# Optimization experiments

Measured on AMD Instinct MI355X. Metric: run time of the kernel, lower is better.

The kernel has to match this reference:

```python
import jax, jax.numpy as jnp
import numpy as np

B, S, EMBED_DIM, FFN_DIM, N_QUBITS = 8, 4096, 768, 3072, 8

# Quantum math: each qubit starts in |0>, gets RX(x_i) then RY(theta_i), then <Z_i>.
# Since all gates are single-qubit, qubits are independent; a short derivation gives
#   <Z_i> = cos(x_i) * cos(theta_i)
# (RX(phi)|0> = (cos(phi/2), -i sin(phi/2)); apply RY(theta); |a|^2-|b|^2 = cos(theta)cos(phi)).

def setup_inputs() -> dict:
    key = jax.random.key(0)
    k1, k2, k3, k4 = jax.random.split(key, 4)
    x = jax.random.normal(k1, (B, S, EMBED_DIM), dtype=jnp.float32)
    theta = jax.random.normal(k2, (N_QUBITS,), dtype=jnp.float32)  # trainable RY angles
    W1 = jax.random.normal(k3, (FFN_DIM, N_QUBITS), dtype=jnp.float32) / np.sqrt(N_QUBITS)
    W2 = jax.random.normal(k4, (EMBED_DIM, FFN_DIM), dtype=jnp.float32) / np.sqrt(FFN_DIM)
    return {"x": x, "theta": theta, "W1": W1, "W2": W2}


def reference(x, theta, W1, W2):
    # RX-encode first N_QUBITS features of each token, RY params, PauliZ expectation.
    # Closed form of the product-state circuit: z[b,s,q] = cos(x[b,s,q]) * cos(theta[q])
    z = jnp.cos(x[..., :N_QUBITS]) * jnp.cos(theta)            # [B, S, Q]
    # dropout is identity in eval mode
    h = jax.nn.relu(jnp.einsum("bsq,fq->bsf", z, W1))          # [B, S, F]
    out = jnp.einsum("bsf,ef->bse", h, W2)                     # [B, S, E]
    return out
```

## Files before the change

kernel.cpp:

```cpp
#include <hip/hip_runtime.h>
#include <hip/hip_bf16.h>
#include <math.h>

#define T_TOK   32768
#define EDIM    768
#define FDIM    3072
#define NQ      8

#define NET     24
#define NKF     192
#define NFT     96
#define NTT     1024

#define NMB     128
#define NPAN    6

#define W2P_BYTES (NKF * NET * 64 * 8 * 2)
#define W1P_BYTES (NFT * 64 * 8 * 2)
#define ZP_BYTES  (NTT * 64 * 8 * 2)
#define W1P_OFFU  (W2P_BYTES / 2)
#define ZP_OFFU   ((W2P_BYTES + W1P_BYTES) / 2)
#define WS_NEED   ((size_t)(W2P_BYTES + W1P_BYTES + ZP_BYTES))

typedef float f32x16 __attribute__((ext_vector_type(16)));
typedef float f32x4  __attribute__((ext_vector_type(4)));
typedef short bf16x8 __attribute__((ext_vector_type(8)));

union FragU { uint4 u; bf16x8 v; };

static __device__ __forceinline__ unsigned pack2(float lo, float hi) {
    unsigned r;
    asm("v_cvt_pk_bf16_f32 %0, %1, %2" : "=v"(r) : "v"(lo), "v"(hi));
    return r;
}

static __device__ __forceinline__ unsigned short f2bf(float f) {
    unsigned int u = __float_as_uint(f);
    unsigned int r = (u + 0x7FFFu + ((u >> 16) & 1u)) >> 16;
    return (unsigned short)r;
}

__global__ __launch_bounds__(256) void ffq_pack(
    const float* __restrict__ x, const float* __restrict__ theta,
    const float* __restrict__ W1, const float* __restrict__ W2,
    unsigned short* __restrict__ ws)
{
    const int bid = blockIdx.x;
    unsigned short* W2P = ws;
    unsigned short* W1P = ws + W1P_OFFU;
    unsigned short* ZP  = ws + ZP_OFFU;

    if (bid < 1152) {
        const int t = bid * 256 + threadIdx.x;
        const int lane = t & 63, fe = t >> 6;
        const int kf = fe / NET, et = fe - kf * NET;
        const int g = lane >> 5, c = lane & 31;
        const int e  = et * 32 + c;
        const int f0 = kf * 16 + g * 4;
        const float4 a = *(const float4*)(W2 + (size_t)e * FDIM + f0);
        const float4 b = *(const float4*)(W2 + (size_t)e * FDIM + f0 + 8);
        FragU u;
        u.u.x = pack2(a.x, a.y); u.u.y = pack2(a.z, a.w);
        u.u.z = pack2(b.x, b.y); u.u.w = pack2(b.z, b.w);
        *(uint4*)(W2P + (((size_t)et * NKF + kf) * 64 + lane) * 8) = u.u;
    } else if (bid < 1176) {
        const int t = (bid - 1152) * 256 + threadIdx.x;
        const int lane = t & 63, ft = t >> 6;
        const int g = lane >> 5, c = lane & 31;
        FragU u; u.u = (uint4){0, 0, 0, 0};
        if (g == 0) {
            const float4 a = *(const float4*)(W1 + (size_t)(ft * 32 + c) * NQ);
            const float4 b = *(const float4*)(W1 + (size_t)(ft * 32 + c) * NQ + 4);
            u.u.x = pack2(a.x, a.y); u.u.y = pack2(a.z, a.w);
            u.u.z = pack2(b.x, b.y); u.u.w = pack2(b.z, b.w);
        }
        *(uint4*)(W1P + (size_t)t * 8) = u.u;
    } else {
        const int t = (bid - 1176) * 256 + threadIdx.x;
        const int lane = t & 63, tt = t >> 6;
        const int g = lane >> 5, c = lane & 31;
        FragU u; u.u = (uint4){0, 0, 0, 0};
        if (g == 0) {
            const int token = tt * 32 + c;
            const float4 a = *(const float4*)(x + (size_t)token * EDIM);
            const float4 b = *(const float4*)(x + (size_t)token * EDIM + 4);
            const float z0 = __cosf(a.x) * __cosf(theta[0]);
            const float z1 = __cosf(a.y) * __cosf(theta[1]);
            const float z2 = __cosf(a.z) * __cosf(theta[2]);
            const float z3 = __cosf(a.w) * __cosf(theta[3]);
            const float z4 = __cosf(b.x) * __cosf(theta[4]);
            const float z5 = __cosf(b.y) * __cosf(theta[5]);
            const float z6 = __cosf(b.z) * __cosf(theta[6]);
            const float z7 = __cosf(b.w) * __cosf(theta[7]);
            u.u.x = pack2(z0, z1); u.u.y = pack2(z2, z3);
            u.u.z = pack2(z4, z5); u.u.w = pack2(z6, z7);
        }
        *(uint4*)(ZP + (size_t)t * 8) = u.u;
    }
}

#define SGB(mask, n) __builtin_amdgcn_sched_group_barrier((mask), (n), 0)

__global__ __launch_bounds__(256, 2) void ffq_main(
    const unsigned short* __restrict__ ws, float* __restrict__ out)
{
    const unsigned short* W1Pp = ws + W1P_OFFU;
    const unsigned short* ZP   = ws + ZP_OFFU;

    const int tid  = threadIdx.x;
    const int wave = tid >> 6;
    const int lane = tid & 63;
    const int g    = lane >> 5;
    const int c    = lane & 31;

    const int sw    = (blockIdx.x & 7) * 96 + (blockIdx.x >> 3);
    const int panel = sw / NMB;
    const int mblk  = sw % NMB;

    const int tt0 = mblk * 8 + wave * 2;
    const int et0 = panel * 4;
    const size_t lo8 = (size_t)lane * 8;

    const bf16x8 zb0 = *(const bf16x8*)(ZP + (size_t)tt0 * 512 + lo8);
    const bf16x8 zb1 = *(const bf16x8*)(ZP + (size_t)(tt0 + 1) * 512 + lo8);

    const unsigned lane16 = (unsigned)lane * 16u;
    const unsigned vo0 = (unsigned)((et0 + 0) * NKF) * 1024u + lane16;
    const unsigned vo1 = (unsigned)((et0 + 1) * NKF) * 1024u + lane16;
    const unsigned vo2 = (unsigned)((et0 + 2) * NKF) * 1024u + lane16;
    const unsigned vo3 = (unsigned)((et0 + 3) * NKF) * 1024u + lane16;
    const char* Wb = (const char*)ws;

    const f32x16 Zc = (f32x16)(0.f);
    f32x16 A00 = Zc, A01 = Zc, A02 = Zc, A03 = Zc;
    f32x16 A10 = Zc, A11 = Zc, A12 = Zc, A13 = Zc;
    f32x16 d0, d1;
    bf16x8 a0l, a0h, a1l, a1h;
    bf16x8 Bl0, Bl1, Bl2, Bl3, Bh0, Bh1, Bh2, Bh3;
    bf16x8 wa;

#define MFMA32(A, B, C) __builtin_amdgcn_mfma_f32_32x32x16_bf16((A), (B), (C), 0, 0, 0)

#define MKAF(d, o) ({                                                    \
        FragU u_;                                                        \
        u_.u.x = pack2(fmaxf((d)[(o)+0], 0.f), fmaxf((d)[(o)+1], 0.f));  \
        u_.u.y = pack2(fmaxf((d)[(o)+2], 0.f), fmaxf((d)[(o)+3], 0.f));  \
        u_.u.z = pack2(fmaxf((d)[(o)+4], 0.f), fmaxf((d)[(o)+5], 0.f));  \
        u_.u.w = pack2(fmaxf((d)[(o)+6], 0.f), fmaxf((d)[(o)+7], 0.f));  \
        u_.v; })

    Bl0 = *(const bf16x8*)(Wb + vo0);        Bh0 = *(const bf16x8*)(Wb + vo0 + 1024);
    Bl1 = *(const bf16x8*)(Wb + vo1);        Bh1 = *(const bf16x8*)(Wb + vo1 + 1024);
    Bl2 = *(const bf16x8*)(Wb + vo2);        Bh2 = *(const bf16x8*)(Wb + vo2 + 1024);
    Bl3 = *(const bf16x8*)(Wb + vo3);        Bh3 = *(const bf16x8*)(Wb + vo3 + 1024);
    wa  = *(const bf16x8*)(W1Pp + lo8);
    d0 = MFMA32(wa, zb0, Zc);
    d1 = MFMA32(wa, zb1, Zc);
    wa  = *(const bf16x8*)(W1Pp + 512 + lo8);
    a0l = MKAF(d0, 0); a0h = MKAF(d0, 8);
    a1l = MKAF(d1, 0); a1h = MKAF(d1, 8);

    #pragma unroll 1
    for (int n = 0; n < NFT; ++n) {
        d0 = MFMA32(wa, zb0, Zc);
        d1 = MFMA32(wa, zb1, Zc);
        wa = *(const bf16x8*)(W1Pp + (size_t)(n + 2) * 512 + lo8);

        A00 = MFMA32(a0l, Bl0, A00); A01 = MFMA32(a0l, Bl1, A01);
        A02 = MFMA32(a0l, Bl2, A02); A03 = MFMA32(a0l, Bl3, A03);
        A10 = MFMA32(a1l, Bl0, A10); A11 = MFMA32(a1l, Bl1, A11);
        A12 = MFMA32(a1l, Bl2, A12); A13 = MFMA32(a1l, Bl3, A13);
        Bl0 = *(const bf16x8*)(Wb + vo0 + 2048);
        Bl1 = *(const bf16x8*)(Wb + vo1 + 2048);
        Bl2 = *(const bf16x8*)(Wb + vo2 + 2048);
        Bl3 = *(const bf16x8*)(Wb + vo3 + 2048);
        a0l = MKAF(d0, 0);
        a1l = MKAF(d1, 0);
        SGB(0x8, 2); SGB(0x20, 1);
        SGB(0x8, 2); SGB(0x20, 1); SGB(0x2, 6);
        SGB(0x8, 2); SGB(0x20, 1); SGB(0x2, 6);
        SGB(0x8, 2); SGB(0x20, 1); SGB(0x2, 6);
        SGB(0x8, 2); SGB(0x20, 1); SGB(0x2, 6);

        A00 = MFMA32(a0h, Bh0, A00); A01 = MFMA32(a0h, Bh1, A01);
        A02 = MFMA32(a0h, Bh2, A02); A03 = MFMA32(a0h, Bh3, A03);
        A10 = MFMA32(a1h, Bh0, A10); A11 = MFMA32(a1h, Bh1, A11);
        A12 = MFMA32(a1h, Bh2, A12); A13 = MFMA32(a1h, Bh3, A13);
        Bh0 = *(const bf16x8*)(Wb + vo0 + 3072);
        Bh1 = *(const bf16x8*)(Wb + vo1 + 3072);
        Bh2 = *(const bf16x8*)(Wb + vo2 + 3072);
        Bh3 = *(const bf16x8*)(Wb + vo3 + 3072);
        a0h = MKAF(d0, 8);
        a1h = MKAF(d1, 8);
        SGB(0x8, 2); SGB(0x20, 1); SGB(0x2, 6);
        SGB(0x8, 2); SGB(0x20, 1); SGB(0x2, 6);
        SGB(0x8, 2); SGB(0x20, 1); SGB(0x2, 6);
        SGB(0x8, 2); SGB(0x20, 1); SGB(0x2, 6);

        Wb += 2048;
    }

#define STORE_ACC(ACC, T, E) do {                                              \
        const size_t rb = (size_t)((tt0 + (T)) * 32 + 4 * g) * EDIM            \
                          + (size_t)(et0 + (E)) * 32 + c;                      \
        _Pragma("unroll")                                                      \
        for (int r = 0; r < 16; ++r)                                           \
            out[rb + (size_t)((r & 3) + 8 * (r >> 2)) * EDIM] = ACC[r];        \
    } while (0)

    STORE_ACC(A00, 0, 0); STORE_ACC(A01, 0, 1); STORE_ACC(A02, 0, 2); STORE_ACC(A03, 0, 3);
    STORE_ACC(A10, 1, 0); STORE_ACC(A11, 1, 1); STORE_ACC(A12, 1, 2); STORE_ACC(A13, 1, 3);

#undef MFMA32
#undef MKAF
#undef STORE_ACC
}

#define BM      128
#define NPANEL  6
#define NMBLK   256
#define BK      64
#define NKSTEP  (FDIM / BK)
#define HA_ST   72
#define BT_ST   72

__global__ __launch_bounds__(256) void ffq_fused(
    const float* __restrict__ x, const float* __restrict__ theta,
    const float* __restrict__ W1, const float* __restrict__ W2,
    float* __restrict__ out)
{
    __shared__ __align__(16) unsigned short hA[BM * HA_ST];
    __shared__ __align__(16) unsigned short Bt[BM * BT_ST];

    const int tid  = threadIdx.x;
    const int wave = tid >> 6;
    const int lane = tid & 63;
    const int l15  = lane & 15;
    const int lhi  = lane >> 4;
    const int wm   = wave >> 1;
    const int wn   = wave & 1;

    const int panel = blockIdx.x / NMBLK;
    const int mblk  = blockIdx.x % NMBLK;
    const int t0 = mblk * BM;
    const int n0 = panel * BM;

    bf16x8 zf[2];
    #pragma unroll
    for (int s = 0; s < 2; ++s) {
        bf16x8 z = {0, 0, 0, 0, 0, 0, 0, 0};
        if (lhi == 0) {
            const int tok = t0 + (wave * 2 + s) * 16 + l15;
            const float4* xp = (const float4*)(x + (size_t)tok * EDIM);
            const float4 x0 = xp[0];
            const float4 x1 = xp[1];
            z[0] = (short)f2bf(cosf(x0.x) * cosf(theta[0]));
            z[1] = (short)f2bf(cosf(x0.y) * cosf(theta[1]));
            z[2] = (short)f2bf(cosf(x0.z) * cosf(theta[2]));
            z[3] = (short)f2bf(cosf(x0.w) * cosf(theta[3]));
            z[4] = (short)f2bf(cosf(x1.x) * cosf(theta[4]));
            z[5] = (short)f2bf(cosf(x1.y) * cosf(theta[5]));
            z[6] = (short)f2bf(cosf(x1.z) * cosf(theta[6]));
            z[7] = (short)f2bf(cosf(x1.w) * cosf(theta[7]));
        }
        zf[s] = z;
    }

    f32x4 acc[4][4];
    #pragma unroll
    for (int mi = 0; mi < 4; ++mi)
        #pragma unroll
        for (int ni = 0; ni < 4; ++ni)
            acc[mi][ni] = (f32x4){0.f, 0.f, 0.f, 0.f};

    for (int ks = 0; ks < NKSTEP; ++ks) {
        const int k0 = ks * BK;
        __syncthreads();
        {
            const int e    = tid >> 1;
            const int half = (tid & 1) * 32;
            const float* src = W2 + (size_t)(n0 + e) * FDIM + k0 + half;
            unsigned short* dst = &Bt[e * BT_ST + half];
            #pragma unroll
            for (int i = 0; i < 4; ++i) {
                const float4 a = ((const float4*)src)[2 * i];
                const float4 b = ((const float4*)src)[2 * i + 1];
                bf16x8 v;
                v[0] = (short)f2bf(a.x); v[1] = (short)f2bf(a.y);
                v[2] = (short)f2bf(a.z); v[3] = (short)f2bf(a.w);
                v[4] = (short)f2bf(b.x); v[5] = (short)f2bf(b.y);
                v[6] = (short)f2bf(b.z); v[7] = (short)f2bf(b.w);
                *(bf16x8*)(dst + i * 8) = v;
            }
        }
        #pragma unroll
        for (int ns = 0; ns < 4; ++ns) {
            bf16x8 wf = {0, 0, 0, 0, 0, 0, 0, 0};
            if (lhi == 0) {
                const float* wp = W1 + (size_t)(k0 + ns * 16 + l15) * NQ;
                const float4 a = ((const float4*)wp)[0];
                const float4 b = ((const float4*)wp)[1];
                wf[0] = (short)f2bf(a.x); wf[1] = (short)f2bf(a.y);
                wf[2] = (short)f2bf(a.z); wf[3] = (short)f2bf(a.w);
                wf[4] = (short)f2bf(b.x); wf[5] = (short)f2bf(b.y);
                wf[6] = (short)f2bf(b.z); wf[7] = (short)f2bf(b.w);
            }
            #pragma unroll
            for (int s = 0; s < 2; ++s) {
                f32x4 hd = __builtin_amdgcn_mfma_f32_16x16x32_bf16(
                    zf[s], wf, (f32x4){0.f, 0.f, 0.f, 0.f}, 0, 0, 0);
                const int row = (wave * 2 + s) * 16 + lhi * 4;
                const int col = ns * 16 + l15;
                #pragma unroll
                for (int j = 0; j < 4; ++j) {
                    const float v = hd[j] > 0.f ? hd[j] : 0.f;
                    hA[(row + j) * HA_ST + col] = f2bf(v);
                }
            }
        }
        __syncthreads();
        #pragma unroll
        for (int ksub = 0; ksub < 2; ++ksub) {
            bf16x8 af[4], bg[4];
            #pragma unroll
            for (int mi = 0; mi < 4; ++mi) {
                const int row = wm * 64 + mi * 16 + l15;
                af[mi] = *(const bf16x8*)&hA[row * HA_ST + ksub * 32 + lhi * 8];
            }
            #pragma unroll
            for (int ni = 0; ni < 4; ++ni) {
                const int e = wn * 64 + ni * 16 + l15;
                bg[ni] = *(const bf16x8*)&Bt[e * BT_ST + ksub * 32 + lhi * 8];
            }
            #pragma unroll
            for (int mi = 0; mi < 4; ++mi)
                #pragma unroll
                for (int ni = 0; ni < 4; ++ni)
                    acc[mi][ni] = __builtin_amdgcn_mfma_f32_16x16x32_bf16(
                        af[mi], bg[ni], acc[mi][ni], 0, 0, 0);
        }
    }

    #pragma unroll
    for (int mi = 0; mi < 4; ++mi) {
        const int rbase = t0 + wm * 64 + mi * 16 + lhi * 4;
        #pragma unroll
        for (int ni = 0; ni < 4; ++ni) {
            const int cc = n0 + wn * 64 + ni * 16 + l15;
            #pragma unroll
            for (int j = 0; j < 4; ++j)
                out[(size_t)(rbase + j) * EDIM + cc] = acc[mi][ni][j];
        }
    }
}

extern "C" void kernel_launch(void* const* d_in, const int* in_sizes, int n_in,
                              void* d_out, int out_size, void* d_ws, size_t ws_size,
                              hipStream_t stream) {
    const float* x     = (const float*)d_in[0];
    const float* theta = (const float*)d_in[1];
    const float* W1    = (const float*)d_in[2];
    const float* W2    = (const float*)d_in[3];
    float* out = (float*)d_out;

    if (ws_size >= WS_NEED) {
        ffq_pack<<<dim3(1432), dim3(256), 0, stream>>>(x, theta, W1, W2,
                                                       (unsigned short*)d_ws);
        ffq_main<<<dim3(NPAN * NMB), dim3(256), 0, stream>>>(
            (const unsigned short*)d_ws, out);
    } else {
        ffq_fused<<<dim3(NPANEL * NMBLK), dim3(256), 0, stream>>>(x, theta, W1, W2, out);
    }
}
```

Measured before the change: 157.0 us.

## Stage W2 and W1 tiles through double-buffered LDS via global_load_lds

Replaces the per-wave direct global loads of W2 B-fragments and W1 fragments with a block-cooperative double-buffered LDS staging scheme using global_load_lds DMA. Each wave loads a quarter of the shared B tiles, and all four waves then read them from LDS. This cuts duplicate global/L2 traffic, since all waves previously fetched identical W2 fragments. In exchange it adds a vmcnt(0) drain plus a block barrier every iteration, which serialises the waves and may expose load latency.

Result: no change. 156.1 us (-0.5%).

```diff
diff --git a/kernel.cpp b/kernel.cpp
--- a/kernel.cpp
+++ b/kernel.cpp
@@ -101,11 +101,21 @@
 
 #define SGB(mask, n) __builtin_amdgcn_sched_group_barrier((mask), (n), 0)
 
+#define SYNC_WITH_DMA_DRAIN() do {                                  \
+        asm volatile("s_waitcnt vmcnt(0)" ::: "memory");            \
+        __builtin_amdgcn_sched_barrier(0);                          \
+        __syncthreads();                                            \
+    } while (0)
+
+#define GLL(gsrc, ldst)                                                        \
+    __builtin_amdgcn_global_load_lds(                                          \
+        (const __attribute__((address_space(1))) unsigned int*)(const void*)(gsrc), \
+        (__attribute__((address_space(3))) unsigned int*)(void*)(ldst), 16, 0, 0)
+
 __global__ __launch_bounds__(256, 2) void ffq_main(
     const unsigned short* __restrict__ ws, float* __restrict__ out)
 {
-    const unsigned short* W1Pp = ws + W1P_OFFU;
-    const unsigned short* ZP   = ws + ZP_OFFU;
+    __shared__ __align__(16) unsigned short Bst[2][9][512];
 
     const int tid  = threadIdx.x;
     const int wave = tid >> 6;
@@ -120,24 +130,29 @@
     const int tt0 = mblk * 8 + wave * 2;
     const int et0 = panel * 4;
     const size_t lo8 = (size_t)lane * 8;
-
+    const unsigned lane16 = (unsigned)lane * 16u;
+
+    const unsigned short* ZP = ws + ZP_OFFU;
     const bf16x8 zb0 = *(const bf16x8*)(ZP + (size_t)tt0 * 512 + lo8);
     const bf16x8 zb1 = *(const bf16x8*)(ZP + (size_t)(tt0 + 1) * 512 + lo8);
 
-    const unsigned lane16 = (unsigned)lane * 16u;
     const unsigned vo0 = (unsigned)((et0 + 0) * NKF) * 1024u + lane16;
     const unsigned vo1 = (unsigned)((et0 + 1) * NKF) * 1024u + lane16;
     const unsigned vo2 = (unsigned)((et0 + 2) * NKF) * 1024u + lane16;
     const unsigned vo3 = (unsigned)((et0 + 3) * NKF) * 1024u + lane16;
-    const char* Wb = (const char*)ws;
+    const char* W2base = (const char*)ws;
+    const char* W1s = (const char*)ws + W2P_BYTES + lane16;
+
+    char* l0 = (char*)&Bst[0][0][0];
+    char* l1 = (char*)&Bst[1][0][0];
+    const unsigned short* r0 = &Bst[0][0][0] + lo8;
+    const unsigned short* r1 = &Bst[1][0][0] + lo8;
 
     const f32x16 Zc = (f32x16)(0.f);
     f32x16 A00 = Zc, A01 = Zc, A02 = Zc, A03 = Zc;
     f32x16 A10 = Zc, A11 = Zc, A12 = Zc, A13 = Zc;
     f32x16 d0, d1;
     bf16x8 a0l, a0h, a1l, a1h;
-    bf16x8 Bl0, Bl1, Bl2, Bl3, Bh0, Bh1, Bh2, Bh3;
-    bf16x8 wa;
 
 #define MFMA32(A, B, C) __builtin_amdgcn_mfma_f32_32x32x16_bf16((A), (B), (C), 0, 0, 0)
 
@@ -149,56 +164,88 @@
         u_.u.w = pack2(fmaxf((d)[(o)+6], 0.f), fmaxf((d)[(o)+7], 0.f));  \
         u_.v; })
 
-    Bl0 = *(const bf16x8*)(Wb + vo0);        Bh0 = *(const bf16x8*)(Wb + vo0 + 1024);
-    Bl1 = *(const bf16x8*)(Wb + vo1);        Bh1 = *(const bf16x8*)(Wb + vo1 + 1024);
-    Bl2 = *(const bf16x8*)(Wb + vo2);        Bh2 = *(const bf16x8*)(Wb + vo2 + 1024);
-    Bl3 = *(const bf16x8*)(Wb + vo3);        Bh3 = *(const bf16x8*)(Wb + vo3 + 1024);
-    wa  = *(const bf16x8*)(W1Pp + lo8);
-    d0 = MFMA32(wa, zb0, Zc);
-    d1 = MFMA32(wa, zb1, Zc);
-    wa  = *(const bf16x8*)(W1Pp + 512 + lo8);
-    a0l = MKAF(d0, 0); a0h = MKAF(d0, 8);
-    a1l = MKAF(d1, 0); a1h = MKAF(d1, 8);
+    if (wave == 0) {
+        GLL(W2base + vo0,        l0 + 0);
+        GLL(W2base + vo0 + 1024, l0 + 4096);
+        GLL(W1s + 1024,          l0 + 8192);
+    } else if (wave == 1) {
+        GLL(W2base + vo1,        l0 + 1024);
+        GLL(W2base + vo1 + 1024, l0 + 5120);
+    } else if (wave == 2) {
+        GLL(W2base + vo2,        l0 + 2048);
+        GLL(W2base + vo2 + 1024, l0 + 6144);
+    } else {
+        GLL(W2base + vo3,        l0 + 3072);
+        GLL(W2base + vo3 + 1024, l0 + 7168);
+    }
+    {
+        const bf16x8 wa0 = *(const bf16x8*)(W1s);
+        d0 = MFMA32(wa0, zb0, Zc);
+        d1 = MFMA32(wa0, zb1, Zc);
+        a0l = MKAF(d0, 0); a0h = MKAF(d0, 8);
+        a1l = MKAF(d1, 0); a1h = MKAF(d1, 8);
+    }
+
+    int wslot = 2048;
+
+#define BODY(RB, LN) do {                                                      \
+        SYNC_WITH_DMA_DRAIN();                                                 \
+        if (wave == 0) {                                                       \
+            GLL(W2base + vo0 + 2048, (LN) + 0);                                \
+            GLL(W2base + vo0 + 3072, (LN) + 4096);                             \
+            GLL(W1s + wslot,         (LN) + 8192);                             \
+        } else if (wave == 1) {                                                \
+            GLL(W2base + vo1 + 2048, (LN) + 1024);                             \
+            GLL(W2base + vo1 + 3072, (LN) + 5120);                             \
+        } else if (wave == 2) {                                                \
+            GLL(W2base + vo2 + 2048, (LN) + 2048);                             \
+            GLL(W2base + vo2 + 3072, (LN) + 6144);                             \
+        } else {                                                               \
+            GLL(W2base + vo3 + 2048, (LN) + 3072);                             \
+            GLL(W2base + vo3 + 3072, (LN) + 7168);                             \
+        }                                                                      \
+        wslot += 1024;                                                         \
+        const bf16x8 wal = *(const bf16x8*)((RB) + 4096);                      \
+        const bf16x8 Bl0 = *(const bf16x8*)((RB) + 0);                         \
+        const bf16x8 Bl1 = *(const bf16x8*)((RB) + 512);                       \
+        const bf16x8 Bl2 = *(const bf16x8*)((RB) + 1024);                      \
+        const bf16x8 Bl3 = *(const bf16x8*)((RB) + 1536);                      \
+        const bf16x8 Bh0 = *(const bf16x8*)((RB) + 2048);                      \
+        const bf16x8 Bh1 = *(const bf16x8*)((RB) + 2560);                      \
+        const bf16x8 Bh2 = *(const bf16x8*)((RB) + 3072);                      \
+        const bf16x8 Bh3 = *(const bf16x8*)((RB) + 3584);                      \
+        d0 = MFMA32(wal, zb0, Zc);                                             \
+        d1 = MFMA32(wal, zb1, Zc);                                             \
+        A00 = MFMA32(a0l, Bl0, A00); A01 = MFMA32(a0l, Bl1, A01);              \
+        A02 = MFMA32(a0l, Bl2, A02); A03 = MFMA32(a0l, Bl3, A03);              \
+        A10 = MFMA32(a1l, Bl0, A10); A11 = MFMA32(a1l, Bl1, A11);              \
+        A12 = MFMA32(a1l, Bl2, A12); A13 = MFMA32(a1l, Bl3, A13);              \
+        A00 = MFMA32(a0h, Bh0, A00); A01 = MFMA32(a0h, Bh1, A01);              \
+        A02 = MFMA32(a0h, Bh2, A02); A03 = MFMA32(a0h, Bh3, A03);              \
+        A10 = MFMA32(a1h, Bh0, A10); A11 = MFMA32(a1h, Bh1, A11);              \
+        A12 = MFMA32(a1h, Bh2, A12); A13 = MFMA32(a1h, Bh3, A13);              \
+        a0l = MKAF(d0, 0);  a1l = MKAF(d1, 0);                                 \
+        a0h = MKAF(d0, 8);  a1h = MKAF(d1, 8);                                 \
+        SGB(0x100, 5);                              \
+        SGB(0x8, 2);                                \
+        SGB(0x100, 4);                              \
+        SGB(0x8, 2); SGB(0x2, 6);                                              \
+        SGB(0x8, 2); SGB(0x2, 6);                                              \
+        SGB(0x8, 2); SGB(0x2, 6);                                              \
+        SGB(0x8, 2); SGB(0x2, 6);                                              \
+        SGB(0x8, 2); SGB(0x2, 6);                                              \
+        SGB(0x8, 2); SGB(0x2, 6);                                              \
+        SGB(0x8, 2); SGB(0x2, 6);                                              \
+        SGB(0x8, 2); SGB(0x2, 6);                                              \
+        W2base += 2048;                                                        \
+    } while (0)
 
     #pragma unroll 1
-    for (int n = 0; n < NFT; ++n) {
-        d0 = MFMA32(wa, zb0, Zc);
-        d1 = MFMA32(wa, zb1, Zc);
-        wa = *(const bf16x8*)(W1Pp + (size_t)(n + 2) * 512 + lo8);
-
-        A00 = MFMA32(a0l, Bl0, A00); A01 = MFMA32(a0l, Bl1, A01);
-        A02 = MFMA32(a0l, Bl2, A02); A03 = MFMA32(a0l, Bl3, A03);
-        A10 = MFMA32(a1l, Bl0, A10); A11 = MFMA32(a1l, Bl1, A11);
-        A12 = MFMA32(a1l, Bl2, A12); A13 = MFMA32(a1l, Bl3, A13);
-        Bl0 = *(const bf16x8*)(Wb + vo0 + 2048);
-        Bl1 = *(const bf16x8*)(Wb + vo1 + 2048);
-        Bl2 = *(const bf16x8*)(Wb + vo2 + 2048);
-        Bl3 = *(const bf16x8*)(Wb + vo3 + 2048);
-        a0l = MKAF(d0, 0);
-        a1l = MKAF(d1, 0);
-        SGB(0x8, 2); SGB(0x20, 1);
-        SGB(0x8, 2); SGB(0x20, 1); SGB(0x2, 6);
-        SGB(0x8, 2); SGB(0x20, 1); SGB(0x2, 6);
-        SGB(0x8, 2); SGB(0x20, 1); SGB(0x2, 6);
-        SGB(0x8, 2); SGB(0x20, 1); SGB(0x2, 6);
-
-        A00 = MFMA32(a0h, Bh0, A00); A01 = MFMA32(a0h, Bh1, A01);
-        A02 = MFMA32(a0h, Bh2, A02); A03 = MFMA32(a0h, Bh3, A03);
-        A10 = MFMA32(a1h, Bh0, A10); A11 = MFMA32(a1h, Bh1, A11);
-        A12 = MFMA32(a1h, Bh2, A12); A13 = MFMA32(a1h, Bh3, A13);
-        Bh0 = *(const bf16x8*)(Wb + vo0 + 3072);
-        Bh1 = *(const bf16x8*)(Wb + vo1 + 3072);
-        Bh2 = *(const bf16x8*)(Wb + vo2 + 3072);
-        Bh3 = *(const bf16x8*)(Wb + vo3 + 3072);
-        a0h = MKAF(d0, 8);
-        a1h = MKAF(d1, 8);
-        SGB(0x8, 2); SGB(0x20, 1); SGB(0x2, 6);
-        SGB(0x8, 2); SGB(0x20, 1); SGB(0x2, 6);
-        SGB(0x8, 2); SGB(0x20, 1); SGB(0x2, 6);
-        SGB(0x8, 2); SGB(0x20, 1); SGB(0x2, 6);
-
-        Wb += 2048;
-    }
+    for (int h = 0; h < NFT / 2; ++h) {
+        BODY(r0, l1);
+        BODY(r1, l0);
+    }
+    SYNC_WITH_DMA_DRAIN();
 
 #define STORE_ACC(ACC, T, E) do {                                              \
         const size_t rb = (size_t)((tt0 + (T)) * 32 + 4 * g) * EDIM            \
@@ -213,6 +260,7 @@
 
 #undef MFMA32
 #undef MKAF
+#undef BODY
 #undef STORE_ACC
 }
 
```
